# Kernel optimization log

Hardware: AMD Instinct MI355X
Metric: run time of the kernel (lower is better)

## Reference

```python
import jax, jax.numpy as jnp
import numpy as np

NH, HD = 12, 64          # heads, head dim (d_model=768)
SC = HD ** -0.5          # both Attention and CA_Attention use head_dim**-0.5


def patchify(x, p1, p2):
    # 'b c (h p1) (w p2) -> b (h w) (p1 p2 c)'
    B, C, H, W = x.shape
    h, w = H // p1, W // p2
    x = x.reshape(B, C, h, p1, w, p2).transpose(0, 2, 4, 3, 5, 1)  # b h w p1 p2 c
    return x.reshape(B, h * w, p1 * p2 * C)


def unpatchify(x, h, w, p1, p2, c):
    # 'b (h w) (p1 p2 c) -> b c (h p1) (w p2)'
    B = x.shape[0]
    x = x.reshape(B, h, w, p1, p2, c).transpose(0, 5, 1, 3, 2, 4)
    return x.reshape(B, c, h * p1, w * p2)


def ln(x, g, b):
    m = x.mean(-1, keepdims=True)
    v = ((x - m) ** 2).mean(-1, keepdims=True)
    return (x - m) / jnp.sqrt(v + 1e-5) * g + b


def setup_inputs() -> dict:
    key = jax.random.key(0)
    specs = [
        ('img_feats', (2, 32, 112, 112, 80)), ('txt', (2, 77, 768)),
        ('pe_w_ax', (1120, 768)), ('pe_b_ax', (768,)),
        ('pe_w_sag', (1120, 768)), ('pe_b_sag', (768,)),
        ('pe_w_cor', (1568, 768)), ('pe_b_cor', (768,)),
        ('pos_ax', (1, 256, 768)), ('pos_sag', (1, 256, 768)), ('pos_cor', (1, 256, 768)),
        ('qw', (768, 768)), ('kw', (768, 768)), ('vw', (768, 768)),
        ('pw', (768, 768)), ('pb', (768,)),
        ('caq_w', (768, 768)), ('caq_b', (768,)), ('cak_w', (768, 768)), ('cak_b', (768,)),
        ('cav_w', (768, 768)), ('cav_b', (768,)), ('cao_w', (768, 768)), ('cao_b', (768,)),
        ('mlp_w1', (768, 3072)), ('mlp_b1', (3072,)), ('mlp_w2', (3072, 768)), ('mlp_b2', (768,)),
        ('ow_ax', (768, 1120)), ('ob_ax', (1120,)),
        ('ow_sag', (768, 1120)), ('ob_sag', (1120,)),
        ('ow_cor', (768, 1568)), ('ob_cor', (1568,)),
    ]
    big = {'img_feats', 'txt', 'pos_ax', 'pos_sag', 'pos_cor'}
    out = {}
    for k, (n, s) in zip(jax.random.split(key, len(specs)), specs):
        scale = 1.0 if n in big else 0.02
        out[n] = jax.random.normal(k, s, jnp.float32) * scale
    out['view_w'] = jnp.ones((3,), jnp.float32)
    for n in ('n1_g', 'n2_g', 'n3_g'):
        out[n] = jnp.ones((768,), jnp.float32)
    for n in ('n1_b', 'n2_b', 'n3_b'):
        out[n] = jnp.zeros((768,), jnp.float32)
    return out


def reference(img_feats, txt, pe_w_ax, pe_b_ax, pe_w_sag, pe_b_sag, pe_w_cor, pe_b_cor,
              pos_ax, pos_sag, pos_cor, view_w, qw, kw, vw, pw, pb,
              caq_w, caq_b, cak_w, cak_b, cav_w, cav_b, cao_w, cao_b,
              n1_g, n1_b, n2_g, n2_b, n3_g, n3_b,
              mlp_w1, mlp_b1, mlp_w2, mlp_b2,
              ow_ax, ob_ax, ow_sag, ob_sag, ow_cor, ob_cor):

    def img_attn(t):
        B, N, C = t.shape
        q = (t @ qw).reshape(B, N, NH, HD)
        k = (t @ kw).reshape(B, N, NH, HD)
        v = (t @ vw).reshape(B, N, NH, HD)
        a = jax.nn.softmax(jnp.einsum('bnkc,bmkc->bknm', q, k) * SC, axis=-1)
        x = jnp.einsum('bknm,bmkc->bnkc', a, v).reshape(B, N, C)
        return x @ pw + pb

    def ca_attn(t, im):
        B, T, _ = t.shape
        N = im.shape[1]
        qh = (t @ caq_w + caq_b).reshape(B, T, NH, HD).transpose(0, 2, 1, 3)
        kh = (im @ cak_w + cak_b).reshape(B, N, NH, HD).transpose(0, 2, 1, 3)
        vh = (im @ cav_w + cav_b).reshape(B, N, NH, HD).transpose(0, 2, 1, 3)
        a = jax.nn.softmax(jnp.einsum('bhid,bhjd->bhij', qh, kh) * SC, axis=-1)
        # faithful to original einsum 'b h i j, b h j d -> b h j d' (sums over i)
        o = jnp.einsum('bhij,bhjd->bhjd', a, vh)
        o = o.transpose(0, 2, 1, 3).reshape(B, N, NH * HD)
        return o @ cao_w + cao_b

    def branch(v2d, pe_w, pe_b, pos, ow, ob, p1, p2):
        B, C, H, W = v2d.shape
        h, w = H // p1, W // p2
        q = patchify(v2d, p1, p2) @ pe_w + pe_b + pos
        q = ln(q, n1_g, n1_b)
        q = q + img_attn(q)
        q = ln(q, n2_g, n2_b)
        x = q + ca_attn(txt, q)
        x = x + (jax.nn.gelu(ln(x, n3_g, n3_b) @ mlp_w1 + mlp_b1, approximate=False) @ mlp_w2 + mlp_b2)
        return unpatchify(x @ ow + ob, h, w, p1, p2, C)

    # adaptive_avg_pool3d to size-1 along one axis == mean over that axis
    ax = img_feats.mean(2)    # (B,C,H,W)
    sag = img_feats.mean(3)   # (B,C,D,W)
    cor = img_feats.mean(4)   # (B,C,D,H)
    oax = branch(ax, pe_w_ax, pe_b_ax, pos_ax, ow_ax, ob_ax, 7, 5)
    osag = branch(sag, pe_w_sag, pe_b_sag, pos_sag, ow_sag, ob_sag, 7, 5)
    ocor = branch(cor, pe_w_cor, pe_b_cor, pos_cor, ow_cor, ob_cor, 7, 7)
    v3 = (view_w[0] * oax[:, :, None] + view_w[1] * osag[:, :, :, None]
          + view_w[2] * ocor[:, :, :, :, None])
    return img_feats + v3
```

## Files before the change

### kernel.cpp

```cpp
#include <hip/hip_runtime.h>
#include <math.h>

typedef __attribute__((ext_vector_type(8))) short s8;
typedef __attribute__((ext_vector_type(4))) float f4;
typedef unsigned short u16;

__device__ inline u16 f2bf(float f) {
    unsigned u = __float_as_uint(f);
    u += 0x7fffu + ((u >> 16) & 1u);
    return (u16)(u >> 16);
}
__device__ inline float bf2f(u16 x) {
    return __uint_as_float(((unsigned)x) << 16);
}
#define MFMA16(a, b, c) __builtin_amdgcn_mfma_f32_16x16x32_bf16(a, b, c, 0, 0, 0)

__global__ __launch_bounds__(256) void mean3_k(const float* __restrict__ img,
                                               float* __restrict__ axp,
                                               float* __restrict__ sag,
                                               float* __restrict__ cor) {
    __shared__ float sl[112*81];
    int blk = blockIdx.x;
    int dc = blk & 15, bc = blk >> 4;
    int d0 = dc * 7;
    int t = threadIdx.x;
    f4 axr[9];
    #pragma unroll
    for (int k = 0; k < 9; ++k) axr[k] = (f4){0.f,0.f,0.f,0.f};
    const float* base = img + (size_t)bc * 1003520 + (size_t)d0 * 8960;
    for (int sidx = 0; sidx < 7; ++sidx) {
        const f4* sp = reinterpret_cast<const f4*>(base + (size_t)sidx * 8960);
        #pragma unroll
        for (int k = 0; k < 9; ++k) {
            int q = t + k * 256;
            if (q < 2240) {
                f4 v = sp[q];
                axr[k] += v;
                int h = q / 20, w4 = q % 20;
                float* row = &sl[h * 81 + w4 * 4];
                row[0] = v[0]; row[1] = v[1]; row[2] = v[2]; row[3] = v[3];
            }
        }
        __syncthreads();
        if (t < 112) {
            float acc = 0.f;
            #pragma unroll 8
            for (int w = 0; w < 80; ++w) acc += sl[t * 81 + w];
            cor[((size_t)bc * 112 + d0 + sidx) * 112 + t] = acc * (1.f / 80.f);
        } else if (t < 192) {
            int w = t - 112;
            float acc = 0.f;
            #pragma unroll 8
            for (int h = 0; h < 112; ++h) acc += sl[h * 81 + w];
            sag[((size_t)bc * 112 + d0 + sidx) * 80 + w] = acc * (1.f / 112.f);
        }
        __syncthreads();
    }
    float* axo = axp + ((size_t)dc * 64 + bc) * 8960;
    #pragma unroll
    for (int k = 0; k < 9; ++k) {
        int q = t + k * 256;
        if (q < 2240) *reinterpret_cast<f4*>(axo + q * 4) = axr[k];
    }
}

struct TT {
    const float* in[16];
    u16* out[16];
    int K[16];
    int N[16];
    int start[16];
};

__global__ __launch_bounds__(256) void transp_all(TT tab) {
    __shared__ float tl[32][33];
    int bid = blockIdx.x;
    int e = 0;
    #pragma unroll
    for (int i = 1; i < 16; ++i) if (bid >= tab.start[i]) e = i;
    const float* in = tab.in[e];
    u16* out = tab.out[e];
    int K = tab.K[e], N = tab.N[e];
    int tid = bid - tab.start[e];
    int nt = N >> 5;
    int k0 = (tid / nt) * 32, n0 = (tid % nt) * 32;
    int t = threadIdx.x;
    int r = t >> 5, c = t & 31;
    #pragma unroll
    for (int i = 0; i < 4; ++i) tl[r + i*8][c] = in[(long)(k0 + r + i*8)*N + n0 + c];
    __syncthreads();
    #pragma unroll
    for (int i = 0; i < 4; ++i) out[(long)(n0 + r + i*8)*K + k0 + c] = f2bf(tl[c][r + i*8]);
}

__global__ __launch_bounds__(256) void patchify3_k(const float* __restrict__ axp,
                                                   const float* __restrict__ m_sag,
                                                   const float* __restrict__ m_cor,
                                                   u16* __restrict__ P0, u16* __restrict__ P1,
                                                   u16* __restrict__ P2) {
    __shared__ float sl[32][113];
    int br = blockIdx.y;
    int X = blockIdx.x;
    int b = X / 112, rem = X % 112;
    int hh = rem / 7, pp1 = rem % 7;
    const float* src; u16* dst; int Wt, p2, PD;
    if (br == 0)      { src = nullptr; dst = P0; Wt = 80;  p2 = 5; PD = 1120; }
    else if (br == 1) { src = m_sag;   dst = P1; Wt = 80;  p2 = 5; PD = 1120; }
    else              { src = m_cor;   dst = P2; Wt = 112; p2 = 7; PD = 1568; }
    int t = threadIdx.x;
    int row = hh*7 + pp1;
    int wq = Wt >> 2;
    if (br == 0) {
        for (int i = t; i < 32*20; i += 256) {
            int c = i / 20, w4 = i % 20;
            f4 s = (f4){0.f,0.f,0.f,0.f};
            size_t base = ((size_t)(b*32 + c)*112 + row)*80 + w4*4;
            #pragma unroll
            for (int p = 0; p < 16; ++p)
                s += *reinterpret_cast<const f4*>(axp + (size_t)p*573440 + base);
            s *= (1.f/112.f);
            sl[c][w4*4+0] = s[0]; sl[c][w4*4+1] = s[1]; sl[c][w4*4+2] = s[2]; sl[c][w4*4+3] = s[3];
        }
    } else {
        for (int i = t; i < 32*wq; i += 256) {
            int c = i / wq, w4 = i % wq;
            float4 v = *reinterpret_cast<const float4*>(
                src + ((size_t)(b*32 + c)*112 + row)*Wt + w4*4);
            sl[c][w4*4+0] = v.x; sl[c][w4*4+1] = v.y; sl[c][w4*4+2] = v.z; sl[c][w4*4+3] = v.w;
        }
    }
    __syncthreads();
    int tot = 16 * p2 * 32;
    for (int o = t; o < tot; o += 256) {
        int ww = o / (p2*32), rest = o % (p2*32);
        int pp2 = rest >> 5, c = rest & 31;
        dst[((size_t)(b*256 + hh*16 + ww))*PD + (pp1*p2 + pp2)*32 + c]
            = f2bf(sl[c][ww*p2 + pp2]);
    }
}

__device__ inline void load_tile(const u16* __restrict__ P, int ld, int nrows, int K,
                                 int r0, int k0, int t, s8 v[4]) {
    #pragma unroll
    for (int i = 0; i < 4; ++i) {
        int chunk = t + i*256;
        int row = chunk >> 4, c8 = (chunk & 15) * 8;
        s8 x;
        #pragma unroll
        for (int q = 0; q < 8; ++q) x[q] = 0;
        if (r0 + row < nrows && k0 + c8 < K)
            x = *reinterpret_cast<const s8*>(P + (long)(r0 + row)*ld + k0 + c8);
        v[i] = x;
    }
}
__device__ inline void load_tile_f32(const float* __restrict__ P, int ld, int nrows, int K,
                                     int r0, int k0, int t, s8 v[4]) {
    #pragma unroll
    for (int i = 0; i < 4; ++i) {
        int chunk = t + i*256;
        int row = chunk >> 4, c8 = (chunk & 15) * 8;
        s8 x;
        #pragma unroll
        for (int q = 0; q < 8; ++q) x[q] = 0;
        if (r0 + row < nrows && k0 + c8 < K) {
            const float* src = P + (long)(r0 + row)*ld + k0 + c8;
            #pragma unroll
            for (int q = 0; q < 8; ++q) x[q] = (short)f2bf(src[q]);
        }
        v[i] = x;
    }
}
__device__ inline void write_tile(u16 (*S)[136], int t, const s8 v[4]) {
    #pragma unroll
    for (int i = 0; i < 4; ++i) {
        int chunk = t + i*256;
        *reinterpret_cast<s8*>(&S[chunk >> 4][(chunk & 15)*8]) = v[i];
    }
}
__device__ inline void mfma_tile(const u16 (*As)[136], const u16 (*Bs)[136],
                                 int wr, int wc, int lane, f4 acc[2][2]) {
    int lrow = lane & 15;
    #pragma unroll
    for (int kh = 0; kh < 4; ++kh) {
        int lk = kh*32 + (lane >> 4) * 8;
        s8 af0 = *reinterpret_cast<const s8*>(&As[wr*32 + lrow][lk]);
        s8 af1 = *reinterpret_cast<const s8*>(&As[wr*32 + 16 + lrow][lk]);
        s8 bg0 = *reinterpret_cast<const s8*>(&Bs[wc*32 + lrow][lk]);
        s8 bg1 = *reinterpret_cast<const s8*>(&Bs[wc*32 + 16 + lrow][lk]);
        acc[0][0] = MFMA16(af0, bg0, acc[0][0]);
        acc[0][1] = MFMA16(af0, bg1, acc[0][1]);
        acc[1][0] = MFMA16(af1, bg0, acc[1][0]);
        acc[1][1] = MFMA16(af1, bg1, acc[1][1]);
    }
}

__global__ __launch_bounds__(256) void gemm_bf(
    const u16* __restrict__ A, const u16* __restrict__ Bt,
    float* __restrict__ Cf, u16* __restrict__ Cb,
    int M, int N, int K,
    const float* __restrict__ bias, const float* __restrict__ resid,
    int act)
{
    __shared__ u16 As[2][64][136];
    __shared__ u16 Bs[2][64][136];
    int t = threadIdx.x;
    int m0 = blockIdx.y * 64, n0 = blockIdx.x * 64;
    int wave = t >> 6, lane = t & 63;
    int wr = wave >> 1, wc = wave & 1;
    f4 acc[2][2];
    #pragma unroll
    for (int m = 0; m < 2; ++m)
        #pragma unroll
        for (int n = 0; n < 2; ++n)
            #pragma unroll
            for (int r = 0; r < 4; ++r) acc[m][n][r] = 0.f;
    int nk = (K + 127) >> 7;
    s8 pa[4], pbv[4];
    load_tile(A, K, M, K, m0, 0, t, pa);
    load_tile(Bt, K, N, K, n0, 0, t, pbv);
    write_tile(As[0], t, pa);
    write_tile(Bs[0], t, pbv);
    __syncthreads();
    for (int kt = 0; kt < nk; ++kt) {
        int cur = kt & 1;
        if (kt + 1 < nk) {
            load_tile(A, K, M, K, m0, (kt+1) << 7, t, pa);
            load_tile(Bt, K, N, K, n0, (kt+1) << 7, t, pbv);
        }
        mfma_tile(As[cur], Bs[cur], wr, wc, lane, acc);
        if (kt + 1 < nk) {
            write_tile(As[cur^1], t, pa);
            write_tile(Bs[cur^1], t, pbv);
        }
        __syncthreads();
    }
    #pragma unroll
    for (int m = 0; m < 2; ++m) {
        int rbase = m0 + wr*32 + m*16 + (lane >> 4) * 4;
        #pragma unroll
        for (int n = 0; n < 2; ++n) {
            int col = n0 + wc*32 + n*16 + (lane & 15);
            if (col >= N) continue;
            #pragma unroll
            for (int r = 0; r < 4; ++r) {
                int row = rbase + r;
                if (row >= M) continue;
                float v = acc[m][n][r];
                if (bias)  v += bias[col];
                if (resid) v += resid[(long)row * N + col];
                if (act == 1) v = 0.5f * v * (1.0f + erff(v * 0.70710678118654752f));
                long ci = (long)row * N + col;
                if (Cf) Cf[ci] = v;
                if (Cb) Cb[ci] = f2bf(v);
            }
        }
    }
}

__global__ __launch_bounds__(256) void gemm_big(
    const u16* __restrict__ A, const u16* __restrict__ Bt,
    u16* __restrict__ Cb, u16* __restrict__ vt,
    int N, int K,
    const float* __restrict__ bias, const float* __restrict__ bias2, int act)
{
    __shared__ u16 As[2][128][72];
    __shared__ u16 Bs[2][128][72];
    int t = threadIdx.x;
    int m0 = blockIdx.y * 128, n0 = blockIdx.x * 128;
    int wave = t >> 6, lane = t & 63;
    int wr = wave >> 1, wc = wave & 1;
    f4 acc[4][4];
    #pragma unroll
    for (int m = 0; m < 4; ++m)
        #pragma unroll
        for (int n = 0; n < 4; ++n)
            #pragma unroll
            for (int r = 0; r < 4; ++r) acc[m][n][r] = 0.f;
    int nk = K >> 6;
    s8 pa[4], pbv[4];
    #pragma unroll
    for (int i = 0; i < 4; ++i) {
        int chunk = t + i*256;
        pa[i]  = *reinterpret_cast<const s8*>(A  + (long)(m0 + (chunk>>3))*K + (chunk&7)*8);
        pbv[i] = *reinterpret_cast<const s8*>(Bt + (long)(n0 + (chunk>>3))*K + (chunk&7)*8);
    }
    #pragma unroll
    for (int i = 0; i < 4; ++i) {
        int chunk = t + i*256;
        *reinterpret_cast<s8*>(&As[0][chunk>>3][(chunk&7)*8]) = pa[i];
        *reinterpret_cast<s8*>(&Bs[0][chunk>>3][(chunk&7)*8]) = pbv[i];
    }
    __syncthreads();
    for (int kt = 0; kt < nk; ++kt) {
        int cur = kt & 1;
        if (kt + 1 < nk) {
            int k0 = (kt+1) << 6;
            #pragma unroll
            for (int i = 0; i < 4; ++i) {
                int chunk = t + i*256;
                pa[i]  = *reinterpret_cast<const s8*>(A  + (long)(m0 + (chunk>>3))*K + k0 + (chunk&7)*8);
                pbv[i] = *reinterpret_cast<const s8*>(Bt + (long)(n0 + (chunk>>3))*K + k0 + (chunk&7)*8);
            }
        }
        #pragma unroll
        for (int kh = 0; kh < 2; ++kh) {
            int lk = kh*32 + (lane >> 4) * 8;
            int lr = lane & 15;
            s8 af[4], bf[4];
            #pragma unroll
            for (int m = 0; m < 4; ++m)
                af[m] = *reinterpret_cast<const s8*>(&As[cur][wr*64 + m*16 + lr][lk]);
            #pragma unroll
            for (int n = 0; n < 4; ++n)
                bf[n] = *reinterpret_cast<const s8*>(&Bs[cur][wc*64 + n*16 + lr][lk]);
            #pragma unroll
            for (int m = 0; m < 4; ++m)
                #pragma unroll
                for (int n = 0; n < 4; ++n)
                    acc[m][n] = MFMA16(af[m], bf[n], acc[m][n]);
        }
        if (kt + 1 < nk) {
            #pragma unroll
            for (int i = 0; i < 4; ++i) {
                int chunk = t + i*256;
                *reinterpret_cast<s8*>(&As[cur^1][chunk>>3][(chunk&7)*8]) = pa[i];
                *reinterpret_cast<s8*>(&Bs[cur^1][chunk>>3][(chunk&7)*8]) = pbv[i];
            }
        }
        __syncthreads();
    }
    #pragma unroll
    for (int m = 0; m < 4; ++m) {
        int rbase = m0 + wr*64 + m*16 + (lane >> 4) * 4;
        #pragma unroll
        for (int n = 0; n < 4; ++n) {
            int col = n0 + wc*64 + n*16 + (lane & 15);
            #pragma unroll
            for (int r = 0; r < 4; ++r) {
                int row = rbase + r;
                float v = acc[m][n][r];
                if (bias) {
                    float bb = bias2 ? ((col < 768) ? bias[col] : bias2[col - 768]) : bias[col];
                    v += bb;
                }
                if (act == 1) v = 0.5f * v * (1.0f + erff(v * 0.70710678118654752f));
                u16 b = f2bf(v);
                Cb[(long)row * N + col] = b;
                if (vt && col >= 1536) {
                    int z = (row >> 8) * 12 + ((col - 1536) >> 6);
                    vt[((long)z * 64 + (col & 63)) * 256 + (row & 255)] = b;
                }
            }
        }
    }
}

struct PeDesc {
    const u16* A[3];
    const u16* Bt[4];
    const float* bias[4];
    const float* pos[3];
    int K[4];
    int M[4];
};

__global__ __launch_bounds__(256) void gemm_pe(PeDesc d, const float* __restrict__ txtf,
                                               float* __restrict__ C, u16* __restrict__ QHb) {
    int z = blockIdx.z;
    int M = d.M[z], K = d.K[z];
    int m0 = blockIdx.y * 64, n0 = blockIdx.x * 64;
    if (m0 >= M) return;
    __shared__ u16 As[2][64][136];
    __shared__ u16 Bs[2][64][136];
    const u16* Bb = d.Bt[z];
    const float* bias = d.bias[z];
    int t = threadIdx.x;
    int wave = t >> 6, lane = t & 63;
    int wr = wave >> 1, wc = wave & 1;
    f4 acc[2][2];
    #pragma unroll
    for (int m = 0; m < 2; ++m)
        #pragma unroll
        for (int n = 0; n < 2; ++n)
            #pragma unroll
            for (int r = 0; r < 4; ++r) acc[m][n][r] = 0.f;
    int nk = (K + 127) >> 7;
    s8 pa[4], pbv[4];
    if (z < 3) load_tile(d.A[z], K, M, K, m0, 0, t, pa);
    else       load_tile_f32(txtf, K, M, K, m0, 0, t, pa);
    load_tile(Bb, K, 768, K, n0, 0, t, pbv);
    write_tile(As[0], t, pa);
    write_tile(Bs[0], t, pbv);
    __syncthreads();
    for (int kt = 0; kt < nk; ++kt) {
        int cur = kt & 1;
        if (kt + 1 < nk) {
            if (z < 3) load_tile(d.A[z], K, M, K, m0, (kt+1) << 7, t, pa);
            else       load_tile_f32(txtf, K, M, K, m0, (kt+1) << 7, t, pa);
            load_tile(Bb, K, 768, K, n0, (kt+1) << 7, t, pbv);
        }
        mfma_tile(As[cur], Bs[cur], wr, wc, lane, acc);
        if (kt + 1 < nk) {
            write_tile(As[cur^1], t, pa);
            write_tile(Bs[cur^1], t, pbv);
        }
        __syncthreads();
    }
    #pragma unroll
    for (int m = 0; m < 2; ++m) {
        int rbase = m0 + wr*32 + m*16 + (lane >> 4) * 4;
        #pragma unroll
        for (int n = 0; n < 2; ++n) {
            int col = n0 + wc*32 + n*16 + (lane & 15);
            #pragma unroll
            for (int r = 0; r < 4; ++r) {
                int row = rbase + r;
                if (row >= M) continue;
                float v = acc[m][n][r] + bias[col];
                if (z < 3) {
                    v += d.pos[z][(long)(row & 255)*768 + col];
                    C[((long)z*512 + row) * 768 + col] = v;
                } else {
                    QHb[(long)row * 768 + col] = f2bf(v);
                }
            }
        }
    }
}

struct OwDesc {
    const u16* Bt[3];
    float* plane[3];
    const float* bias[3];
    int N[3];
    int p2[3];
    int Wd[3];
};

__global__ __launch_bounds__(256) void gemm_ow(OwDesc d, const u16* __restrict__ A,
                                               const float* __restrict__ vwp) {
    int z = blockIdx.z;
    int N = d.N[z];
    int n0 = blockIdx.x * 64;
    if (n0 >= N) return;
    __shared__ u16 As[2][64][136];
    __shared__ u16 Bs[2][64][136];
    const u16* Ab = A + (long)z * 512 * 768;
    const u16* Bb = d.Bt[z];
    int t = threadIdx.x;
    int m0 = blockIdx.y * 64;
    int wave = t >> 6, lane = t & 63;
    int wr = wave >> 1, wc = wave & 1;
    f4 acc[2][2];
    #pragma unroll
    for (int m = 0; m < 2; ++m)
        #pragma unroll
        for (int n = 0; n < 2; ++n)
            #pragma unroll
            for (int r = 0; r < 4; ++r) acc[m][n][r] = 0.f;
    s8 pa[4], pbv[4];
    load_tile(Ab, 768, 512, 768, m0, 0, t, pa);
    load_tile(Bb, 768, N, 768, n0, 0, t, pbv);
    write_tile(As[0], t, pa);
    write_tile(Bs[0], t, pbv);
    __syncthreads();
    for (int kt = 0; kt < 6; ++kt) {
        int cur = kt & 1;
        if (kt + 1 < 6) {
            load_tile(Ab, 768, 512, 768, m0, (kt+1) << 7, t, pa);
            load_tile(Bb, 768, N, 768, n0, (kt+1) << 7, t, pbv);
        }
        mfma_tile(As[cur], Bs[cur], wr, wc, lane, acc);
        if (kt + 1 < 6) {
            write_tile(As[cur^1], t, pa);
            write_tile(Bs[cur^1], t, pbv);
        }
        __syncthreads();
    }
    float* plane = d.plane[z];
    const float* bias = d.bias[z];
    int p2 = d.p2[z], Wd = d.Wd[z];
    float wt = vwp[z];
    #pragma unroll
    for (int m = 0; m < 2; ++m) {
        int rbase = m0 + wr*32 + m*16 + (lane >> 4) * 4;
        #pragma unroll
        for (int n = 0; n < 2; ++n) {
            int col = n0 + wc*32 + n*16 + (lane & 15);
            if (col >= N) continue;
            int pp = col >> 5, c = col & 31;
            int pp1 = pp / p2, pp2 = pp % p2;
            float bv = bias[col];
            #pragma unroll
            for (int r = 0; r < 4; ++r) {
                int row = rbase + r;
                int b = row >> 8, nn = row & 255;
                int hh = nn >> 4, ww = nn & 15;
                int ho = hh*7 + pp1, wo = ww*p2 + pp2;
                plane[((long)(b*32 + c)*112 + ho)*Wd + wo] = wt * (acc[m][n][r] + bv);
            }
        }
    }
}

__global__ __launch_bounds__(256) void ln_k(const float* __restrict__ in,
                                            float* __restrict__ outf,
                                            u16* __restrict__ outb,
                                            const float* __restrict__ g,
                                            const float* __restrict__ bta) {
    constexpr int N = 768;
    int row = blockIdx.x;
    const float* x = in + (size_t)row * N;
    int t = threadIdx.x;
    float v0 = x[t], v1 = x[t+256], v2 = x[t+512];
    float s = v0+v1+v2, s2 = v0*v0+v1*v1+v2*v2;
    #pragma unroll
    for (int off = 32; off > 0; off >>= 1) { s += __shfl_down(s, off); s2 += __shfl_down(s2, off); }
    __shared__ float red[8];
    int wid = t >> 6, lane = t & 63;
    if (lane == 0) { red[wid] = s; red[wid+4] = s2; }
    __syncthreads();
    if (t == 0) {
        float S = red[0]+red[1]+red[2]+red[3];
        float S2 = red[4]+red[5]+red[6]+red[7];
        float mean = S * (1.f/N);
        float var = S2 * (1.f/N) - mean*mean;
        red[0] = mean; red[1] = rsqrtf(var + 1e-5f);
    }
    __syncthreads();
    float mean = red[0], rstd = red[1];
    float y0 = (v0-mean)*rstd*g[t]     + bta[t];
    float y1 = (v1-mean)*rstd*g[t+256] + bta[t+256];
    float y2 = (v2-mean)*rstd*g[t+512] + bta[t+512];
    if (outf) {
        float* y = outf + (size_t)row * N;
        y[t] = y0; y[t+256] = y1; y[t+512] = y2;
    }
    if (outb) {
        u16* y = outb + (size_t)row * N;
        y[t] = f2bf(y0); y[t+256] = f2bf(y1); y[t+512] = f2bf(y2);
    }
}

__global__ __launch_bounds__(256) void attn_k(const u16* __restrict__ QKV,
                                              const u16* __restrict__ Vt,
                                              u16* __restrict__ O) {
    __shared__ u16 Ks[256][72];
    __shared__ u16 Ps[128][264];
    __shared__ u16 Vs[64][264];
    int zz = blockIdx.x;
    int bh = zz >> 1, half = zz & 1;
    int bb = bh / 12, h = bh % 12;
    long qrow0 = (long)bb*256 + half*128;
    int hcol = h*64;
    int t = threadIdx.x;
    int wave = t >> 6, lane = t & 63;
    int lr = lane & 15, lg = lane >> 4;
    #pragma unroll
    for (int i = 0; i < 8; ++i) {
        int chunk = t + i*256;
        int row = chunk >> 3, c8 = (chunk & 7)*8;
        *reinterpret_cast<s8*>(&Ks[row][c8]) =
            *reinterpret_cast<const s8*>(QKV + ((long)bb*256 + row)*2304 + 768 + hcol + c8);
    }
    #pragma unroll
    for (int i = 0; i < 8; ++i) {
        int chunk = t + i*256;
        int d = chunk >> 5, j8 = (chunk & 31)*8;
        *reinterpret_cast<s8*>(&Vs[d][j8]) =
            *reinterpret_cast<const s8*>(Vt + (long)bh*16384 + (long)d*256 + j8);
    }
    __syncthreads();
    f4 acc[2][16];
    #pragma unroll
    for (int m = 0; m < 2; ++m)
        #pragma unroll
        for (int n = 0; n < 16; ++n)
            #pragma unroll
            for (int r = 0; r < 4; ++r) acc[m][n][r] = 0.f;
    #pragma unroll
    for (int kh = 0; kh < 2; ++kh) {
        s8 af0 = *reinterpret_cast<const s8*>(QKV + (qrow0 + wave*32 + lr)*2304 + hcol + kh*32 + lg*8);
        s8 af1 = *reinterpret_cast<const s8*>(QKV + (qrow0 + wave*32 + 16 + lr)*2304 + hcol + kh*32 + lg*8);
        #pragma unroll
        for (int n = 0; n < 16; ++n) {
            s8 bf = *reinterpret_cast<const s8*>(&Ks[n*16 + lr][kh*32 + lg*8]);
            acc[0][n] = MFMA16(af0, bf, acc[0][n]);
            acc[1][n] = MFMA16(af1, bf, acc[1][n]);
        }
    }
    #pragma unroll
    for (int m = 0; m < 2; ++m)
        #pragma unroll
        for (int r = 0; r < 4; ++r) {
            float mx = -1e30f;
            #pragma unroll
            for (int n = 0; n < 16; ++n) mx = fmaxf(mx, acc[m][n][r]);
            #pragma unroll
            for (int o = 8; o; o >>= 1) mx = fmaxf(mx, __shfl_xor(mx, o));
            float l = 0.f;
            float p[16];
            #pragma unroll
            for (int n = 0; n < 16; ++n) {
                p[n] = __expf((acc[m][n][r] - mx) * 0.125f);
                l += p[n];
            }
            #pragma unroll
            for (int o = 8; o; o >>= 1) l += __shfl_xor(l, o);
            float inv = 1.f / l;
            int prow = wave*32 + m*16 + lg*4 + r;
            #pragma unroll
            for (int n = 0; n < 16; ++n)
                Ps[prow][n*16 + lr] = f2bf(p[n] * inv);
        }
    __syncthreads();
    f4 o2[2][4];
    #pragma unroll
    for (int m = 0; m < 2; ++m)
        #pragma unroll
        for (int n = 0; n < 4; ++n)
            #pragma unroll
            for (int r = 0; r < 4; ++r) o2[m][n][r] = 0.f;
    #pragma unroll
// ... 112 lines not shown
                #pragma unroll
                for (int n = 0; n < 4; ++n)
                    wn[n] += __expf((acc[m][n][r] - mi) * 0.125f) * inv;
            }
        }
    #pragma unroll
    for (int n = 0; n < 4; ++n) {
        wn[n] += __shfl_xor(wn[n], 16);
        wn[n] += __shfl_xor(wn[n], 32);
    }
    if (lane < 16) {
        #pragma unroll
        for (int n = 0; n < 4; ++n) Wj[wave*64 + n*16 + lr] = wn[n];
    }
    __syncthreads();
    int d = t & 63;
    #pragma unroll 4
    for (int it = 0; it < 64; ++it) {
        int j = it*4 + (t >> 6);
        long row = (long)rowblk*256 + j;
        float vh = bf2f(KVHb[row*1536 + 768 + h*64 + d]);
        O[row*768 + h*64 + d] = f2bf(Wj[j] * vh);
    }
}

__global__ __launch_bounds__(256) void final_k(const float* __restrict__ img,
                                               const float* __restrict__ Aax,
                                               const float* __restrict__ Asag,
                                               const float* __restrict__ Acor,
                                               float* __restrict__ out) {
    int blk = blockIdx.x;
    int bc = blk / 112;
    const float4* ip = reinterpret_cast<const float4*>(img + (size_t)blk * 8960);
    const float4* ap = reinterpret_cast<const float4*>(Aax + (size_t)bc * 8960);
    const float4* sp = reinterpret_cast<const float4*>(Asag + (size_t)blk * 80);
    const float*  cp = Acor + (size_t)blk * 112;
    float4* op = reinterpret_cast<float4*>(out + (size_t)blk * 8960);
    int t = threadIdx.x;
    for (int q = t; q < 2240; q += 256) {
        int h = q / 20, w4 = q % 20;
        float4 iv = ip[q], av = ap[q], sv = sp[w4];
        float cv = cp[h];
        float4 o;
        o.x = iv.x + av.x + sv.x + cv;
        o.y = iv.y + av.y + sv.y + cv;
        o.z = iv.z + av.z + sv.z + cv;
        o.w = iv.w + av.w + sv.w + cv;
        op[q] = o;
    }
}

extern "C" void kernel_launch(void* const* d_in, const int* in_sizes, int n_in,
                              void* d_out, int out_size, void* d_ws, size_t ws_size,
                              hipStream_t stream) {
    (void)in_sizes; (void)n_in; (void)out_size; (void)ws_size;
    const float* img    = (const float*)d_in[0];
    const float* txt    = (const float*)d_in[1];
    const float* pe_w[3] = {(const float*)d_in[2], (const float*)d_in[4], (const float*)d_in[6]};
    const float* pe_b[3] = {(const float*)d_in[3], (const float*)d_in[5], (const float*)d_in[7]};
    const float* pos[3]  = {(const float*)d_in[8], (const float*)d_in[9], (const float*)d_in[10]};
    const float* qw = (const float*)d_in[11];
    const float* kw = (const float*)d_in[12];
    const float* vw_attn = (const float*)d_in[13];
    const float* pw = (const float*)d_in[14];
    const float* pb = (const float*)d_in[15];
    const float* caq_w = (const float*)d_in[16];
    const float* caq_b = (const float*)d_in[17];
    const float* cak_w = (const float*)d_in[18];
    const float* cak_b = (const float*)d_in[19];
    const float* cav_w = (const float*)d_in[20];
    const float* cav_b = (const float*)d_in[21];
    const float* cao_w = (const float*)d_in[22];
    const float* cao_b = (const float*)d_in[23];
    const float* mlp_w1 = (const float*)d_in[24];
    const float* mlp_b1 = (const float*)d_in[25];
    const float* mlp_w2 = (const float*)d_in[26];
    const float* mlp_b2 = (const float*)d_in[27];
    const float* ow[3] = {(const float*)d_in[28], (const float*)d_in[30], (const float*)d_in[32]};
    const float* ob[3] = {(const float*)d_in[29], (const float*)d_in[31], (const float*)d_in[33]};
    const float* view_w = (const float*)d_in[34];
    const float* n_g[3] = {(const float*)d_in[35], (const float*)d_in[36], (const float*)d_in[37]};
    const float* n_b[3] = {(const float*)d_in[38], (const float*)d_in[39], (const float*)d_in[40]};

    unsigned char* sb = (unsigned char*)d_out;
    size_t off = 0;
    auto B = [&](size_t bytes) -> void* {
        void* p = sb + off; off += (bytes + 511) & ~(size_t)511; return p;
    };
    u16* qkvT  = (u16*)B((size_t)2304*768*2);
    u16* pwT   = (u16*)B(768*768*2);
    u16* caqT  = (u16*)B(768*768*2);
    u16* cakvT = (u16*)B((size_t)1536*768*2);
    u16* caoT  = (u16*)B(768*768*2);
    u16* mlp1T = (u16*)B((size_t)3072*768*2);
    u16* mlp2T = (u16*)B((size_t)768*3072*2);
    u16* peT[3]; peT[0] = (u16*)B((size_t)768*1120*2); peT[1] = (u16*)B((size_t)768*1120*2); peT[2] = (u16*)B((size_t)768*1568*2);
    u16* owT[3]; owT[0] = (u16*)B((size_t)1120*768*2); owT[1] = (u16*)B((size_t)1120*768*2); owT[2] = (u16*)B((size_t)1568*768*2);
    float* axp   = (float*)B((size_t)16*573440*4);
    float* m_sag = (float*)B(573440*4);
    float* m_cor = (float*)B(802816*4);
    u16* P0 = (u16*)B((size_t)512*1120*2);
    u16* P1 = (u16*)B((size_t)512*1120*2);
    u16* P2 = (u16*)B((size_t)512*1568*2);
    float* X0  = (float*)B((size_t)1536*768*4);
    float* X1f = (float*)B((size_t)1536*768*4);
    float* X2  = (float*)B((size_t)1536*768*4);
    float* X3f = (float*)B((size_t)1536*768*4);
    float* X4  = (float*)B((size_t)1536*768*4);
    u16* X1b = (u16*)B((size_t)1536*768*2);
    u16* X3b = (u16*)B((size_t)1536*768*2);
    u16* X5b = (u16*)B((size_t)1536*768*2);
    u16* X6b = (u16*)B((size_t)1536*768*2);
    u16* QKVb = (u16*)B((size_t)1536*2304*2);
    u16* Obf = (u16*)B((size_t)1536*768*2);
    u16* Vt  = (u16*)B((size_t)72*64*256*2);
    u16* Hb  = (u16*)B((size_t)1536*3072*2);
    u16* KVHb = (u16*)B((size_t)1536*1536*2);
    u16* QHb  = (u16*)B((size_t)154*768*2);

    float* ws = (float*)d_ws;
    float* Aax  = ws;
    float* Asag = ws + 573440;
    float* Acor = ws + 1146880;

    TT tab;
    {
        const float* ins[16] = {qw, kw, vw_attn, pw, caq_w, cak_w, cav_w, cao_w,
                                mlp_w1, mlp_w2, pe_w[0], pe_w[1], pe_w[2], ow[0], ow[1], ow[2]};
        u16* outs[16] = {qkvT, qkvT + 768*768, qkvT + 2*768*768, pwT, caqT, cakvT,
                         cakvT + 768*768, caoT, mlp1T, mlp2T, peT[0], peT[1], peT[2],
                         owT[0], owT[1], owT[2]};
        int Ks[16] = {768,768,768,768,768,768,768,768, 768,3072, 1120,1120,1568, 768,768,768};
        int Ns[16] = {768,768,768,768,768,768,768,768, 3072,768, 768,768,768, 1120,1120,1568};
        int st = 0;
        for (int i = 0; i < 16; ++i) {
            tab.in[i] = ins[i]; tab.out[i] = outs[i]; tab.K[i] = Ks[i]; tab.N[i] = Ns[i];
            tab.start[i] = st;
            st += (Ks[i] >> 5) * (Ns[i] >> 5);
        }
        transp_all<<<st, 256, 0, stream>>>(tab);
    }

    mean3_k<<<1024, 256, 0, stream>>>(img, axp, m_sag, m_cor);
    patchify3_k<<<dim3(224,3), 256, 0, stream>>>(axp, m_sag, m_cor, P0, P1, P2);

    auto gemm = [&](const u16* A, const u16* Bt, float* Cf, u16* Cb,
                    int M, int N, int K, const float* bias, const float* resid, int act) {
        dim3 g((N+63)/64, (M+63)/64, 1);
        gemm_bf<<<g, 256, 0, stream>>>(A, Bt, Cf, Cb, M, N, K, bias, resid, act);
    };

    {
        PeDesc d;
        d.A[0] = P0; d.A[1] = P1; d.A[2] = P2;
        d.Bt[0] = peT[0]; d.Bt[1] = peT[1]; d.Bt[2] = peT[2]; d.Bt[3] = caqT;
        d.bias[0] = pe_b[0]; d.bias[1] = pe_b[1]; d.bias[2] = pe_b[2]; d.bias[3] = caq_b;
        d.pos[0] = pos[0]; d.pos[1] = pos[1]; d.pos[2] = pos[2];
        d.K[0] = 1120; d.K[1] = 1120; d.K[2] = 1568; d.K[3] = 768;
        d.M[0] = 512; d.M[1] = 512; d.M[2] = 512; d.M[3] = 154;
        gemm_pe<<<dim3(12,8,4), 256, 0, stream>>>(d, txt, X0, QHb);
    }

    ln_k<<<1536, 256, 0, stream>>>(X0, X1f, X1b, n_g[0], n_b[0]);
    gemm_big<<<dim3(18,12), 256, 0, stream>>>(X1b, qkvT, QKVb, Vt, 2304, 768, nullptr, nullptr, 0);
    attn_k<<<144, 256, 0, stream>>>(QKVb, Vt, Obf);
    gemm(Obf, pwT, X2, nullptr, 1536, 768, 768, pb, X1f, 0);
    ln_k<<<1536, 256, 0, stream>>>(X2, X3f, X3b, n_g[1], n_b[1]);
    gemm_big<<<dim3(12,12), 256, 0, stream>>>(X3b, cakvT, KVHb, nullptr, 1536, 768, cak_b, cav_b, 0);
    ca_fused<<<72, 256, 0, stream>>>(QHb, KVHb, Obf);
    gemm(Obf, caoT, X4, nullptr, 1536, 768, 768, cao_b, X3f, 0);
    ln_k<<<1536, 256, 0, stream>>>(X4, nullptr, X5b, n_g[2], n_b[2]);
    gemm_big<<<dim3(24,12), 256, 0, stream>>>(X5b, mlp1T, Hb, nullptr, 3072, 768, mlp_b1, nullptr, 1);
    gemm(Hb, mlp2T, nullptr, X6b, 1536, 768, 3072, mlp_b2, X4, 0);
    {
        OwDesc d;
        d.Bt[0] = owT[0]; d.Bt[1] = owT[1]; d.Bt[2] = owT[2];
        d.plane[0] = Aax; d.plane[1] = Asag; d.plane[2] = Acor;
        d.bias[0] = ob[0]; d.bias[1] = ob[1]; d.bias[2] = ob[2];
        d.N[0] = 1120; d.N[1] = 1120; d.N[2] = 1568;
        d.p2[0] = 5; d.p2[1] = 5; d.p2[2] = 7;
        d.Wd[0] = 80; d.Wd[1] = 80; d.Wd[2] = 112;
        gemm_ow<<<dim3(25,8,3), 256, 0, stream>>>(d, X6b, view_w);
    }

    final_k<<<7168, 256, 0, stream>>>(img, Aax, Asag, Acor, (float*)d_out);
}
```

Before: 445.9 us.

## Fuse LayerNorm into GEMM prologues via atomic row stats; merge prep kernels

Result: slower. 485.0 us (+8.8%).

```diff
diff --git a/kernel.cpp b/kernel.cpp
--- a/kernel.cpp
+++ b/kernel.cpp
@@ -14,55 +14,6 @@
     return __uint_as_float(((unsigned)x) << 16);
 }
 #define MFMA16(a, b, c) __builtin_amdgcn_mfma_f32_16x16x32_bf16(a, b, c, 0, 0, 0)
-
-__global__ __launch_bounds__(256) void mean3_k(const float* __restrict__ img,
-                                               float* __restrict__ axp,
-                                               float* __restrict__ sag,
-                                               float* __restrict__ cor) {
-    __shared__ float sl[112*81];
-    int blk = blockIdx.x;
-    int dc = blk & 15, bc = blk >> 4;
-    int d0 = dc * 7;
-    int t = threadIdx.x;
-    f4 axr[9];
-    #pragma unroll
-    for (int k = 0; k < 9; ++k) axr[k] = (f4){0.f,0.f,0.f,0.f};
-    const float* base = img + (size_t)bc * 1003520 + (size_t)d0 * 8960;
-    for (int sidx = 0; sidx < 7; ++sidx) {
-        const f4* sp = reinterpret_cast<const f4*>(base + (size_t)sidx * 8960);
-        #pragma unroll
-        for (int k = 0; k < 9; ++k) {
-            int q = t + k * 256;
-            if (q < 2240) {
-                f4 v = sp[q];
-                axr[k] += v;
-                int h = q / 20, w4 = q % 20;
-                float* row = &sl[h * 81 + w4 * 4];
-                row[0] = v[0]; row[1] = v[1]; row[2] = v[2]; row[3] = v[3];
-            }
-        }
-        __syncthreads();
-        if (t < 112) {
-            float acc = 0.f;
-            #pragma unroll 8
-            for (int w = 0; w < 80; ++w) acc += sl[t * 81 + w];
-            cor[((size_t)bc * 112 + d0 + sidx) * 112 + t] = acc * (1.f / 80.f);
-        } else if (t < 192) {
-            int w = t - 112;
-            float acc = 0.f;
-            #pragma unroll 8
-            for (int h = 0; h < 112; ++h) acc += sl[h * 81 + w];
-            sag[((size_t)bc * 112 + d0 + sidx) * 80 + w] = acc * (1.f / 112.f);
-        }
-        __syncthreads();
-    }
-    float* axo = axp + ((size_t)dc * 64 + bc) * 8960;
-    #pragma unroll
-    for (int k = 0; k < 9; ++k) {
-        int q = t + k * 256;
-        if (q < 2240) *reinterpret_cast<f4*>(axo + q * 4) = axr[k];
-    }
-}
 
 struct TT {
     const float* in[16];
@@ -70,27 +21,81 @@
     int K[16];
     int N[16];
     int start[16];
+    int total;
 };
 
-__global__ __launch_bounds__(256) void transp_all(TT tab) {
-    __shared__ float tl[32][33];
+__global__ __launch_bounds__(256) void prep_k(TT tab, const float* __restrict__ img,
+                                              float* __restrict__ axp,
+                                              float* __restrict__ sag,
+                                              float* __restrict__ cor,
+                                              float* __restrict__ stats) {
+    __shared__ float sl[112*81];
     int bid = blockIdx.x;
-    int e = 0;
-    #pragma unroll
-    for (int i = 1; i < 16; ++i) if (bid >= tab.start[i]) e = i;
-    const float* in = tab.in[e];
-    u16* out = tab.out[e];
-    int K = tab.K[e], N = tab.N[e];
-    int tid = bid - tab.start[e];
-    int nt = N >> 5;
-    int k0 = (tid / nt) * 32, n0 = (tid % nt) * 32;
     int t = threadIdx.x;
-    int r = t >> 5, c = t & 31;
-    #pragma unroll
-    for (int i = 0; i < 4; ++i) tl[r + i*8][c] = in[(long)(k0 + r + i*8)*N + n0 + c];
-    __syncthreads();
-    #pragma unroll
-    for (int i = 0; i < 4; ++i) out[(long)(n0 + r + i*8)*K + k0 + c] = f2bf(tl[c][r + i*8]);
+    if (bid < 1024) {
+        int dc = bid & 15, bc = bid >> 4;
+        int d0 = dc * 7;
+        f4 axr[9];
+        #pragma unroll
+        for (int k = 0; k < 9; ++k) axr[k] = (f4){0.f,0.f,0.f,0.f};
+        const float* base = img + (size_t)bc * 1003520 + (size_t)d0 * 8960;
+        for (int sidx = 0; sidx < 7; ++sidx) {
+            const f4* sp = reinterpret_cast<const f4*>(base + (size_t)sidx * 8960);
+            #pragma unroll
+            for (int k = 0; k < 9; ++k) {
+                int q = t + k * 256;
+                if (q < 2240) {
+                    f4 v = sp[q];
+                    axr[k] += v;
+                    int h = q / 20, w4 = q % 20;
+                    float* row = &sl[h * 81 + w4 * 4];
+                    row[0] = v[0]; row[1] = v[1]; row[2] = v[2]; row[3] = v[3];
+                }
+            }
+            __syncthreads();
+            if (t < 112) {
+                float acc = 0.f;
+                #pragma unroll 8
+                for (int w = 0; w < 80; ++w) acc += sl[t * 81 + w];
+                cor[((size_t)bc * 112 + d0 + sidx) * 112 + t] = acc * (1.f / 80.f);
+            } else if (t < 192) {
+                int w = t - 112;
+                float acc = 0.f;
+                #pragma unroll 8
+                for (int h = 0; h < 112; ++h) acc += sl[h * 81 + w];
+                sag[((size_t)bc * 112 + d0 + sidx) * 80 + w] = acc * (1.f / 112.f);
+            }
+            __syncthreads();
+        }
+        float* axo = axp + ((size_t)dc * 64 + bc) * 8960;
+        #pragma unroll
+        for (int k = 0; k < 9; ++k) {
+            int q = t + k * 256;
+            if (q < 2240) *reinterpret_cast<f4*>(axo + q * 4) = axr[k];
+        }
+        return;
+    }
+    int tb = bid - 1024;
+    if (tb < tab.total) {
+        float (*tl)[33] = reinterpret_cast<float(*)[33]>(sl);
+        int e = 0;
+        #pragma unroll
+        for (int i = 1; i < 16; ++i) if (tb >= tab.start[i]) e = i;
+        const float* in = tab.in[e];
+        u16* out = tab.out[e];
+        int K = tab.K[e], N = tab.N[e];
+        int tid = tb - tab.start[e];
+        int nt = N >> 5;
+        int k0 = (tid / nt) * 32, n0 = (tid % nt) * 32;
+        int r = t >> 5, c = t & 31;
+        #pragma unroll
+        for (int i = 0; i < 4; ++i) tl[r + i*8][c] = in[(long)(k0 + r + i*8)*N + n0 + c];
+        __syncthreads();
+        #pragma unroll
+        for (int i = 0; i < 4; ++i) out[(long)(n0 + r + i*8)*K + k0 + c] = f2bf(tl[c][r + i*8]);
+        return;
+    }
+    for (int i = t; i < 9216; i += 256) stats[i] = 0.f;
 }
 
 __global__ __launch_bounds__(256) void patchify3_k(const float* __restrict__ axp,
@@ -193,12 +198,21 @@
         acc[1][1] = MFMA16(af1, bg1, acc[1][1]);
     }
 }
+__device__ inline void ln_params(const float* stats, int row, float& mean, float& rstd) {
+    float su = stats[row*2], sq = stats[row*2+1];
+    mean = su * (1.f/768.f);
+    rstd = rsqrtf(sq * (1.f/768.f) - mean*mean + 1e-5f);
+}
 
 __global__ __launch_bounds__(256) void gemm_bf(
     const u16* __restrict__ A, const u16* __restrict__ Bt,
     float* __restrict__ Cf, u16* __restrict__ Cb,
     int M, int N, int K,
-    const float* __restrict__ bias, const float* __restrict__ resid,
+    const float* __restrict__ bias,
+    const float* __restrict__ resid,
+    const float* __restrict__ rstats, const float* __restrict__ rg,
+    const float* __restrict__ rb,
+    float* __restrict__ stats_out,
     int act)
 {
     __shared__ u16 As[2][64][136];
@@ -207,6 +221,7 @@
     int m0 = blockIdx.y * 64, n0 = blockIdx.x * 64;
     int wave = t >> 6, lane = t & 63;
     int wr = wave >> 1, wc = wave & 1;
+    int lr = lane & 15;
     f4 acc[2][2];
     #pragma unroll
     for (int m = 0; m < 2; ++m)
@@ -234,12 +249,17 @@
         }
         __syncthreads();
     }
+    float ps[2][4], psq[2][4];
+    #pragma unroll
+    for (int m = 0; m < 2; ++m)
+        #pragma unroll
+        for (int r = 0; r < 4; ++r) { ps[m][r] = 0.f; psq[m][r] = 0.f; }
     #pragma unroll
     for (int m = 0; m < 2; ++m) {
         int rbase = m0 + wr*32 + m*16 + (lane >> 4) * 4;
         #pragma unroll
         for (int n = 0; n < 2; ++n) {
-            int col = n0 + wc*32 + n*16 + (lane & 15);
+            int col = n0 + wc*32 + n*16 + lr;
             if (col >= N) continue;
             #pragma unroll
             for (int r = 0; r < 4; ++r) {
@@ -247,24 +267,54 @@
                 if (row >= M) continue;
                 float v = acc[m][n][r];
                 if (bias)  v += bias[col];
-                if (resid) v += resid[(long)row * N + col];
+                if (rstats) {
+                    float mean, rstd;
+                    ln_params(rstats, row, mean, rstd);
+                    v += (resid[(long)row * N + col] - mean) * rstd * rg[col] + rb[col];
+                } else if (resid) {
+                    v += resid[(long)row * N + col];
+                }
                 if (act == 1) v = 0.5f * v * (1.0f + erff(v * 0.70710678118654752f));
                 long ci = (long)row * N + col;
                 if (Cf) Cf[ci] = v;
                 if (Cb) Cb[ci] = f2bf(v);
+                ps[m][r] += v; psq[m][r] += v*v;
+            }
+        }
+    }
+    if (stats_out) {
+        #pragma unroll
+        for (int m = 0; m < 2; ++m) {
+            int rbase = m0 + wr*32 + m*16 + (lane >> 4) * 4;
+            #pragma unroll
+            for (int r = 0; r < 4; ++r) {
+                float p = ps[m][r], q = psq[m][r];
+                #pragma unroll
+                for (int o = 1; o < 16; o <<= 1) {
+                    p += __shfl_xor(p, o);
+                    q += __shfl_xor(q, o);
+                }
+                if (lr == 0) {
+                    int row = rbase + r;
+                    if (row < M) {
+                        atomicAdd(&stats_out[row*2],   p);
+                        atomicAdd(&stats_out[row*2+1], q);
+                    }
+                }
             }
         }
     }
 }
 
 __global__ __launch_bounds__(256) void gemm_big(
-    const u16* __restrict__ A, const u16* __restrict__ Bt,
-    u16* __restrict__ Cb, u16* __restrict__ vt,
-    int N, int K,
-    const float* __restrict__ bias, const float* __restrict__ bias2, int act)
+    const float* __restrict__ A32, const float* __restrict__ astats,
+    const float* __restrict__ ag, const float* __restrict__ ab,
+    const u16* __restrict__ Bt, u16* __restrict__ Cb, u16* __restrict__ vt,
+    int N, const float* __restrict__ bias, const float* __restrict__ bias2, int act)
 {
     __shared__ u16 As[2][128][72];
     __shared__ u16 Bs[2][128][72];
+    constexpr int K = 768;
     int t = threadIdx.x;
     int m0 = blockIdx.y * 128, n0 = blockIdx.x * 128;
     int wave = t >> 6, lane = t & 63;
@@ -276,12 +326,24 @@
         for (int n = 0; n < 4; ++n)
             #pragma unroll
             for (int r = 0; r < 4; ++r) acc[m][n][r] = 0.f;
-    int nk = K >> 6;
     s8 pa[4], pbv[4];
+    auto loadA = [&](int k0, int i) -> s8 {
+        int chunk = t + i*256;
+        int row = m0 + (chunk>>3);
+        int kk = k0 + (chunk&7)*8;
+        float mean, rstd;
+        ln_params(astats, row, mean, rstd);
+        const float* src = A32 + (long)row*K + kk;
+        s8 x;
+        #pragma unroll
+        for (int q = 0; q < 8; ++q)
+            x[q] = (short)f2bf((src[q]-mean)*rstd*ag[kk+q] + ab[kk+q]);
+        return x;
+    };
     #pragma unroll
     for (int i = 0; i < 4; ++i) {
         int chunk = t + i*256;
-        pa[i]  = *reinterpret_cast<const s8*>(A  + (long)(m0 + (chunk>>3))*K + (chunk&7)*8);
+        pa[i]  = loadA(0, i);
         pbv[i] = *reinterpret_cast<const s8*>(Bt + (long)(n0 + (chunk>>3))*K + (chunk&7)*8);
     }
     #pragma unroll
@@ -291,14 +353,14 @@
         *reinterpret_cast<s8*>(&Bs[0][chunk>>3][(chunk&7)*8]) = pbv[i];
     }
     __syncthreads();
-    for (int kt = 0; kt < nk; ++kt) {
+    for (int kt = 0; kt < 12; ++kt) {
         int cur = kt & 1;
-        if (kt + 1 < nk) {
+        if (kt + 1 < 12) {
             int k0 = (kt+1) << 6;
             #pragma unroll
             for (int i = 0; i < 4; ++i) {
                 int chunk = t + i*256;
-                pa[i]  = *reinterpret_cast<const s8*>(A  + (long)(m0 + (chunk>>3))*K + k0 + (chunk&7)*8);
+                pa[i]  = loadA(k0, i);
                 pbv[i] = *reinterpret_cast<const s8*>(Bt + (long)(n0 + (chunk>>3))*K + k0 + (chunk&7)*8);
             }
         }
@@ -319,7 +381,7 @@
                 for (int n = 0; n < 4; ++n)
                     acc[m][n] = MFMA16(af[m], bf[n], acc[m][n]);
         }
-        if (kt + 1 < nk) {
+        if (kt + 1 < 12) {
             #pragma unroll
             for (int i = 0; i < 4; ++i) {
                 int chunk = t + i*256;
@@ -365,7 +427,8 @@
 };
 
 __global__ __launch_bounds__(256) void gemm_pe(PeDesc d, const float* __restrict__ txtf,
-                                               float* __restrict__ C, u16* __restrict__ QHb) {
+                                               float* __restrict__ C, u16* __restrict__ QHb,
+                                               float* __restrict__ stats1) {
     int z = blockIdx.z;
     int M = d.M[z], K = d.K[z];
     int m0 = blockIdx.y * 64, n0 = blockIdx.x * 64;
@@ -377,6 +440,7 @@
     int t = threadIdx.x;
     int wave = t >> 6, lane = t & 63;
     int wr = wave >> 1, wc = wave & 1;
+    int lr = lane & 15;
     f4 acc[2][2];
     #pragma unroll
     for (int m = 0; m < 2; ++m)
@@ -406,12 +470,17 @@
         }
         __syncthreads();
     }
+    float ps[2][4], psq[2][4];
+    #pragma unroll
+    for (int m = 0; m < 2; ++m)
+        #pragma unroll
+        for (int r = 0; r < 4; ++r) { ps[m][r] = 0.f; psq[m][r] = 0.f; }
     #pragma unroll
     for (int m = 0; m < 2; ++m) {
         int rbase = m0 + wr*32 + m*16 + (lane >> 4) * 4;
         #pragma unroll
         for (int n = 0; n < 2; ++n) {
-            int col = n0 + wc*32 + n*16 + (lane & 15);
+            int col = n0 + wc*32 + n*16 + lr;
             #pragma unroll
             for (int r = 0; r < 4; ++r) {
                 int row = rbase + r;
@@ -420,8 +489,29 @@
                 if (z < 3) {
                     v += d.pos[z][(long)(row & 255)*768 + col];
                     C[((long)z*512 + row) * 768 + col] = v;
+                    ps[m][r] += v; psq[m][r] += v*v;
                 } else {
                     QHb[(long)row * 768 + col] = f2bf(v);
+                }
+            }
+        }
+    }
+    if (z < 3) {
+        #pragma unroll
+        for (int m = 0; m < 2; ++m) {
+            int rbase = m0 + wr*32 + m*16 + (lane >> 4) * 4;
+            #pragma unroll
+            for (int r = 0; r < 4; ++r) {
+                float p = ps[m][r], q = psq[m][r];
+                #pragma unroll
+                for (int o = 1; o < 16; o <<= 1) {
+                    p += __shfl_xor(p, o);
+                    q += __shfl_xor(q, o);
+                }
+                if (lr == 0) {
+                    int grow = z*512 + rbase + r;
+                    atomicAdd(&stats1[grow*2],   p);
+                    atomicAdd(&stats1[grow*2+1], q);
                 }
             }
         }
@@ -496,49 +586,10 @@
                 int row = rbase + r;
                 int b = row >> 8, nn = row & 255;
                 int hh = nn >> 4, ww = nn & 15;
-                int ho = hh*7 + pp1, wo = ww*p2 + pp2;
-                plane[((long)(b*32 + c)*112 + ho)*Wd + wo] = wt * (acc[m][n][r] + bv);
-            }
-        }
-    }
-}
-
-__global__ __launch_bounds__(256) void ln_k(const float* __restrict__ in,
-                                            float* __restrict__ outf,
-                                            u16* __restrict__ outb,
-                                            const float* __restrict__ g,
-                                            const float* __restrict__ bta) {
-    constexpr int N = 768;
-    int row = blockIdx.x;
-    const float* x = in + (size_t)row * N;
-    int t = threadIdx.x;
-    float v0 = x[t], v1 = x[t+256], v2 = x[t+512];
-    float s = v0+v1+v2, s2 = v0*v0+v1*v1+v2*v2;
-    #pragma unroll
-    for (int off = 32; off > 0; off >>= 1) { s += __shfl_down(s, off); s2 += __shfl_down(s2, off); }
-    __shared__ float red[8];
-    int wid = t >> 6, lane = t & 63;
-    if (lane == 0) { red[wid] = s; red[wid+4] = s2; }
-    __syncthreads();
-    if (t == 0) {
-        float S = red[0]+red[1]+red[2]+red[3];
-        float S2 = red[4]+red[5]+red[6]+red[7];
-        float mean = S * (1.f/N);
-        float var = S2 * (1.f/N) - mean*mean;
-        red[0] = mean; red[1] = rsqrtf(var + 1e-5f);
-    }
-    __syncthreads();
-    float mean = red[0], rstd = red[1];
-    float y0 = (v0-mean)*rstd*g[t]     + bta[t];
-    float y1 = (v1-mean)*rstd*g[t+256] + bta[t+256];
-    float y2 = (v2-mean)*rstd*g[t+512] + bta[t+512];
-    if (outf) {
-        float* y = outf + (size_t)row * N;
-        y[t] = y0; y[t+256] = y1; y[t+512] = y2;
-    }
-    if (outb) {
-        u16* y = outb + (size_t)row * N;
-        y[t] = f2bf(y0); y[t+256] = f2bf(y1); y[t+512] = f2bf(y2);
+                plane[((long)(b*32 + c)*112 + hh*7 + pp1)*Wd + ww*p2 + pp2]
+                    = wt * (acc[m][n][r] + bv);
+            }
+        }
     }
 }
 
@@ -817,41 +868,41 @@
     const float* n_g[3] = {(const float*)d_in[35], (const float*)d_in[36], (const float*)d_in[37]};
     const float* n_b[3] = {(const float*)d_in[38], (const float*)d_in[39], (const float*)d_in[40]};
 
+    typedef unsigned short u16t;
     unsigned char* sb = (unsigned char*)d_out;
     size_t off = 0;
     auto B = [&](size_t bytes) -> void* {
         void* p = sb + off; off += (bytes + 511) & ~(size_t)511; return p;
     };
-    u16* qkvT  = (u16*)B((size_t)2304*768*2);
-    u16* pwT   = (u16*)B(768*768*2);
-    u16* caqT  = (u16*)B(768*768*2);
-    u16* cakvT = (u16*)B((size_t)1536*768*2);
-    u16* caoT  = (u16*)B(768*768*2);
-    u16* mlp1T = (u16*)B((size_t)3072*768*2);
-    u16* mlp2T = (u16*)B((size_t)768*3072*2);
-    u16* peT[3]; peT[0] = (u16*)B((size_t)768*1120*2); peT[1] = (u16*)B((size_t)768*1120*2); peT[2] = (u16*)B((size_t)768*1568*2);
-    u16* owT[3]; owT[0] = (u16*)B((size_t)1120*768*2); owT[1] = (u16*)B((size_t)1120*768*2); owT[2] = (u16*)B((size_t)1568*768*2);
+    u16t* qkvT  = (u16t*)B((size_t)2304*768*2);
+    u16t* pwT   = (u16t*)B(768*768*2);
+    u16t* caqT  = (u16t*)B(768*768*2);
+    u16t* cakvT = (u16t*)B((size_t)1536*768*2);
+    u16t* caoT  = (u16t*)B(768*768*2);
+    u16t* mlp1T = (u16t*)B((size_t)3072*768*2);
+    u16t* mlp2T = (u16t*)B((size_t)768*3072*2);
+    u16t* peT[3]; peT[0] = (u16t*)B((size_t)768*1120*2); peT[1] = (u16t*)B((size_t)768*1120*2); peT[2] = (u16t*)B((size_t)768*1568*2);
+    u16t* owT[3]; owT[0] = (u16t*)B((size_t)1120*768*2); owT[1] = (u16t*)B((size_t)1120*768*2); owT[2] = (u16t*)B((size_t)1568*768*2);
     float* axp   = (float*)B((size_t)16*573440*4);
     float* m_sag = (float*)B(573440*4);
     float* m_cor = (float*)B(802816*4);
-    u16* P0 = (u16*)B((size_t)512*1120*2);
-    u16* P1 = (u16*)B((size_t)512*1120*2);
-    u16* P2 = (u16*)B((size_t)512*1568*2);
+    u16t* P0 = (u16t*)B((size_t)512*1120*2);
+    u16t* P1 = (u16t*)B((size_t)512*1120*2);
+    u16t* P2 = (u16t*)B((size_t)512*1568*2);
     float* X0  = (float*)B((size_t)1536*768*4);
-    float* X1f = (float*)B((size_t)1536*768*4);
     float* X2  = (float*)B((size_t)1536*768*4);
-    float* X3f = (float*)B((size_t)1536*768*4);
     float* X4  = (float*)B((size_t)1536*768*4);
-    u16* X1b = (u16*)B((size_t)1536*768*2);
-    u16* X3b = (u16*)B((size_t)1536*768*2);
-    u16* X5b = (u16*)B((size_t)1536*768*2);
-    u16* X6b = (u16*)B((size_t)1536*768*2);
-    u16* QKVb = (u16*)B((size_t)1536*2304*2);
-    u16* Obf = (u16*)B((size_t)1536*768*2);
-    u16* Vt  = (u16*)B((size_t)72*64*256*2);
-    u16* Hb  = (u16*)B((size_t)1536*3072*2);
-    u16* KVHb = (u16*)B((size_t)1536*1536*2);
-    u16* QHb  = (u16*)B((size_t)154*768*2);
+    u16t* X6b = (u16t*)B((size_t)1536*768*2);
+    u16t* QKVb = (u16t*)B((size_t)1536*2304*2);
+    u16t* Obf = (u16t*)B((size_t)1536*768*2);
+    u16t* Vt  = (u16t*)B((size_t)72*64*256*2);
+    u16t* Hb  = (u16t*)B((size_t)1536*3072*2);
+    u16t* KVHb = (u16t*)B((size_t)1536*1536*2);
+    u16t* QHb  = (u16t*)B((size_t)154*768*2);
+    float* stats = (float*)B((size_t)3*1536*2*4);
+    float* stats1 = stats;
+    float* stats2 = stats + 1536*2;
+    float* stats3 = stats + 2*1536*2;
 
     float* ws = (float*)d_ws;
     float* Aax  = ws;
@@ -862,9 +913,9 @@
     {
         const float* ins[16] = {qw, kw, vw_attn, pw, caq_w, cak_w, cav_w, cao_w,
                                 mlp_w1, mlp_w2, pe_w[0], pe_w[1], pe_w[2], ow[0], ow[1], ow[2]};
-        u16* outs[16] = {qkvT, qkvT + 768*768, qkvT + 2*768*768, pwT, caqT, cakvT,
-                         cakvT + 768*768, caoT, mlp1T, mlp2T, peT[0], peT[1], peT[2],
-                         owT[0], owT[1], owT[2]};
+        u16t* outs[16] = {qkvT, qkvT + 768*768, qkvT + 2*768*768, pwT, caqT, cakvT,
+                          cakvT + 768*768, caoT, mlp1T, mlp2T, peT[0], peT[1], peT[2],
+                          owT[0], owT[1], owT[2]};
         int Ks[16] = {768,768,768,768,768,768,768,768, 768,3072, 1120,1120,1568, 768,768,768};
         int Ns[16] = {768,768,768,768,768,768,768,768, 3072,768, 768,768,768, 1120,1120,1568};
         int st = 0;
@@ -873,17 +924,11 @@
             tab.start[i] = st;
             st += (Ks[i] >> 5) * (Ns[i] >> 5);
         }
-        transp_all<<<st, 256, 0, stream>>>(tab);
-    }
-
-    mean3_k<<<1024, 256, 0, stream>>>(img, axp, m_sag, m_cor);
+        tab.total = st;
+        prep_k<<<1024 + st + 1, 256, 0, stream>>>(tab, img, axp, m_sag, m_cor, stats);
+    }
+
     patchify3_k<<<dim3(224,3), 256, 0, stream>>>(axp, m_sag, m_cor, P0, P1, P2);
-
-    auto gemm = [&](const u16* A, const u16* Bt, float* Cf, u16* Cb,
-                    int M, int N, int K, const float* bias, const float* resid, int act) {
-        dim3 g((N+63)/64, (M+63)/64, 1);
-        gemm_bf<<<g, 256, 0, stream>>>(A, Bt, Cf, Cb, M, N, K, bias, resid, act);
-    };
 
     {
         PeDesc d;
@@ -893,20 +938,23 @@
         d.pos[0] = pos[0]; d.pos[1] = pos[1]; d.pos[2] = pos[2];
         d.K[0] = 1120; d.K[1] = 1120; d.K[2] = 1568; d.K[3] = 768;
         d.M[0] = 512; d.M[1] = 512; d.M[2] = 512; d.M[3] = 154;
-        gemm_pe<<<dim3(12,8,4), 256, 0, stream>>>(d, txt, X0, QHb);
-    }
-
-    ln_k<<<1536, 256, 0, stream>>>(X0, X1f, X1b, n_g[0], n_b[0]);
-    gemm_big<<<dim3(18,12), 256, 0, stream>>>(X1b, qkvT, QKVb, Vt, 2304, 768, nullptr, nullptr, 0);
+        gemm_pe<<<dim3(12,8,4), 256, 0, stream>>>(d, txt, X0, QHb, stats1);
+    }
+
+    gemm_big<<<dim3(18,12), 256, 0, stream>>>(X0, stats1, n_g[0], n_b[0],
+                                              qkvT, QKVb, Vt, 2304, nullptr, nullptr, 0);
     attn_k<<<144, 256, 0, stream>>>(QKVb, Vt, Obf);
-    gemm(Obf, pwT, X2, nullptr, 1536, 768, 768, pb, X1f, 0);
-    ln_k<<<1536, 256, 0, stream>>>(X2, X3f, X3b, n_g[1], n_b[1]);
-    gemm_big<<<dim3(12,12), 256, 0, stream>>>(X3b, cakvT, KVHb, nullptr, 1536, 768, cak_b, cav_b, 0);
+    gemm_bf<<<dim3(12,24), 256, 0, stream>>>(Obf, pwT, X2, nullptr, 1536, 768, 768,
+                                             pb, X0, stats1, n_g[0], n_b[0], stats2, 0);
+    gemm_big<<<dim3(12,12), 256, 0, stream>>>(X2, stats2, n_g[1], n_b[1],
+                                              cakvT, KVHb, nullptr, 1536, cak_b, cav_b, 0);
     ca_fused<<<72, 256, 0, stream>>>(QHb, KVHb, Obf);
-    gemm(Obf, caoT, X4, nullptr, 1536, 768, 768, cao_b, X3f, 0);
-    ln_k<<<1536, 256, 0, stream>>>(X4, nullptr, X5b, n_g[2], n_b[2]);
-    gemm_big<<<dim3(24,12), 256, 0, stream>>>(X5b, mlp1T, Hb, nullptr, 3072, 768, mlp_b1, nullptr, 1);
-    gemm(Hb, mlp2T, nullptr, X6b, 1536, 768, 3072, mlp_b2, X4, 0);
+    gemm_bf<<<dim3(12,24), 256, 0, stream>>>(Obf, caoT, X4, nullptr, 1536, 768, 768,
+                                             cao_b, X2, stats2, n_g[1], n_b[1], stats3, 0);
+    gemm_big<<<dim3(24,12), 256, 0, stream>>>(X4, stats3, n_g[2], n_b[2],
+                                              mlp1T, Hb, nullptr, 3072, mlp_b1, nullptr, 1);
+    gemm_bf<<<dim3(12,24), 256, 0, stream>>>(Hb, mlp2T, nullptr, X6b, 1536, 768, 3072,
+                                             mlp_b2, X4, nullptr, nullptr, nullptr, nullptr, 0);
     {
         OwDesc d;
         d.Bt[0] = owT[0]; d.Bt[1] = owT[1]; d.Bt[2] = owT[2];
```
